# Performance work log

Hardware: AMD Instinct MI355X
Metric: run time of the kernel (lower is better)

Reference implementation:

```python
import jax, jax.numpy as jnp
import numpy as np

B, L, DIM, H, D = 4, 1024, 1024, 8, 32


def setup_inputs() -> dict:
    key = jax.random.key(0)
    ks = jax.random.split(key, 8)
    s = 0.02
    return dict(
        x=jax.random.normal(ks[0], (B, L, DIM), jnp.float32),
        W_in=jax.random.normal(ks[1], (DIM, DIM), jnp.float32) * s,
        b_in=jnp.zeros((DIM,), jnp.float32),
        W_qkva=jax.random.normal(ks[2], (H * D * 8, DIM), jnp.float32) * s,
        b_qkva=jnp.zeros((H * D * 8,), jnp.float32),
        W_y=jax.random.normal(ks[3], (DIM, H * D * 2), jnp.float32) * s,
        b_y=jnp.zeros((DIM,), jnp.float32),
        W_out=jax.random.normal(ks[4], (DIM, DIM), jnp.float32) * s,
        b_out=jnp.zeros((DIM,), jnp.float32),
        h0_re=jax.random.normal(ks[5], (H, D, D), jnp.float32),
        h0_im=jax.random.normal(ks[6], (H, D, D), jnp.float32),
    )


def reference(x, W_in, b_in, W_qkva, b_qkva, W_y, b_y, W_out, b_out, h0_re, h0_im):
    b, Ls, dim = x.shape
    Hh, Dd = h0_re.shape[0], h0_re.shape[1]
    u = jax.nn.silu(x @ W_in.T + b_in)
    qkva = (u @ W_qkva.T + b_qkva).reshape(b, Ls, Hh, Dd, 4, 2)
    c = jax.lax.complex(qkva[..., 0], qkva[..., 1])  # [b,L,H,D,4] complex
    q, k, v, a = c[..., 0], c[..., 1], c[..., 2], c[..., 3]
    mag2 = a.real * a.real + a.imag * a.imag
    # unit-modulus rotation scaled by sigmoid(log|a|^2) gate
    a = a * (jax.lax.rsqrt(mag2) * jax.nn.sigmoid(jnp.log(mag2)))
    kv = jnp.einsum('blhd,blhe->blhde', k, v)  # [b,L,H,D,D] complex
    h0 = jax.lax.complex(h0_re, h0_im)[None]  # [1,H,D,D]
    # fold initial state into step 0: h_0 = a_0 * h_init + kv_0
    kv = kv.at[:, 0].add(a[:, 0, ..., None] * h0)
    a_e = a[..., None]  # [b,L,H,D,1], broadcasts over state col dim

    def comb(c1, c2):
        a1, x1 = c1
        a2, x2 = c2
        return (a1 * a2, a2 * x1 + x2)

    # linear recurrence h_l = a_l * h_{l-1} + kv_l (equiv. to the FFT/cumsum
    # triangular-product matrix in the original module)
    _, h = jax.lax.associative_scan(comb, (a_e, kv), axis=1)
    y = jnp.einsum('blhd,blhde->blhe', q, h)  # [b,L,H,D] complex
    y2 = jnp.stack([y.real, y.imag], axis=-1).reshape(b, Ls, Hh * Dd * 2)
    y2 = jax.nn.silu(y2 @ W_y.T + b_y)
    return y2 @ W_out.T + b_out
```

## Files before the change

### kernel.cpp

```cpp
#include <hip/hip_runtime.h>

#define B_ 4
#define L_ 1024
#define DIM_ 1024
#define H_ 8
#define D_ 32
#define LSEG 16
#define NSEG (L_/LSEG)

typedef __bf16 bf16_t;
typedef __bf16 bf16x8 __attribute__((ext_vector_type(8)));
typedef float f32x4 __attribute__((ext_vector_type(4)));

__device__ __forceinline__ void gload_lds16(const bf16_t* g, bf16_t* l) {
  __builtin_amdgcn_global_load_lds((const __attribute__((address_space(1))) void*)g,
                                   (__attribute__((address_space(3))) void*)l, 16, 0, 0);
}
__device__ __forceinline__ void gload_lds16f(const float* g, float* l) {
  __builtin_amdgcn_global_load_lds((const __attribute__((address_space(1))) void*)g,
                                   (__attribute__((address_space(3))) void*)l, 16, 0, 0);
}

__global__ __launch_bounds__(256) void cvt_all(const float* __restrict__ x,
                                               const float* __restrict__ w1,
                                               const float* __restrict__ w2,
                                               const float* __restrict__ w3,
                                               const float* __restrict__ w4,
                                               bf16_t* __restrict__ ox,
                                               bf16_t* __restrict__ o1,
                                               bf16_t* __restrict__ o2,
                                               bf16_t* __restrict__ o3,
                                               bf16_t* __restrict__ o4) {
  int g = blockIdx.x;
  const float* in; bf16_t* out; int i;
  if      (g < 4096) { in = x;  out = ox; i = g * 256 + threadIdx.x; }
  else if (g < 5120) { in = w1; out = o1; i = (g - 4096) * 256 + threadIdx.x; }
  else if (g < 7168) { in = w2; out = o2; i = (g - 5120) * 256 + threadIdx.x; }
  else if (g < 7680) { in = w3; out = o3; i = (g - 7168) * 256 + threadIdx.x; }
  else               { in = w4; out = o4; i = (g - 7680) * 256 + threadIdx.x; }
  float4 v = ((const float4*)in)[i];
  union { bf16_t b[4]; unsigned long long q; } pk;
  pk.b[0] = (bf16_t)v.x; pk.b[1] = (bf16_t)v.y;
  pk.b[2] = (bf16_t)v.z; pk.b[3] = (bf16_t)v.w;
  ((unsigned long long*)out)[i] = pk.q;
}

template<int BN, int ACT, int OUTBF, int GATE, int TRANS>
__global__ __launch_bounds__(256) void gemm_nt(const bf16_t* __restrict__ A,
                                               const bf16_t* __restrict__ Bm,
                                               const float* __restrict__ bias,
                                               void* __restrict__ Cout,
                                               int M, int N, int K) {
  constexpr int NI = BN / 32;
  constexpr int ISS_B = BN / 32;
  __shared__ __align__(16) bf16_t As[128 * 64];
  __shared__ __align__(16) bf16_t Bs[BN * 64];
  const int t = threadIdx.x;
  const int wid = t >> 6, lane = t & 63;
  const int wr = wid >> 1, wc = wid & 1;
  const int lr = lane & 15, lq = lane >> 4;
  const int bm = blockIdx.x, bn = blockIdx.y;
  const int rA = wid * 32 + (lane >> 3);
  const int rB = wid * (BN / 4) + (lane >> 3);
  const int c8 = (((lane & 7) ^ ((lane >> 3) & 7))) * 8;
  const bf16_t* Ag = A + (size_t)(bm * 128 + rA) * K + c8;
  const bf16_t* Bg = Bm + (size_t)(bn * BN + rB) * K + c8;
  bf16_t* AsW = As + (wid * 32) * 64;
  bf16_t* BsW = Bs + (wid * (BN / 4)) * 64;
  f32x4 acc[4][NI] = {};
  for (int k0 = 0; k0 < K; k0 += 64) {
#pragma unroll
    for (int j = 0; j < 4; ++j)
      gload_lds16(Ag + (size_t)j * 8 * K, AsW + j * 8 * 64);
#pragma unroll
    for (int j = 0; j < ISS_B; ++j)
      gload_lds16(Bg + (size_t)j * 8 * K, BsW + j * 8 * 64);
    Ag += 64; Bg += 64;
    __syncthreads();
#pragma unroll
    for (int ks = 0; ks < 2; ++ks) {
      const int sg = ks * 4 + lq;
      const int sl = (sg ^ (lr & 7)) * 8;
      bf16x8 af[4], bfv[NI];
#pragma unroll
      for (int mi = 0; mi < 4; ++mi)
        af[mi] = *(const bf16x8*)&As[(wr * 64 + mi * 16 + lr) * 64 + sl];
#pragma unroll
      for (int ni = 0; ni < NI; ++ni)
        bfv[ni] = *(const bf16x8*)&Bs[(wc * (BN/2) + ni * 16 + lr) * 64 + sl];
#pragma unroll
      for (int mi = 0; mi < 4; ++mi)
#pragma unroll
        for (int ni = 0; ni < NI; ++ni)
          acc[mi][ni] = __builtin_amdgcn_mfma_f32_16x16x32_bf16(af[mi], bfv[ni], acc[mi][ni], 0, 0, 0);
    }
    __syncthreads();
  }
#pragma unroll
  for (int mi = 0; mi < 4; ++mi) {
#pragma unroll
    for (int ni = 0; ni < NI; ++ni) {
      int colg = bn * BN + wc * (BN/2) + ni * 16 + lr;
      float bb = bias[colg];
#pragma unroll
      for (int r = 0; r < 4; ++r) {
        int rowg = bm * 128 + wr * 64 + mi * 16 + lq * 4 + r;
        float v = acc[mi][ni][r] + bb;
        if (ACT == 1) v = v / (1.0f + __expf(-v));
        if (GATE) {
          float wv = __shfl_xor(v, 1);
          if ((colg & 7) >= 6) {
            float m2 = v * v + wv * wv;
            v *= sqrtf(m2) / (1.0f + m2);
          }
        }
        if (TRANS) {
          size_t idx = (((size_t)((rowg >> 10) * 8 + (colg >> 8))) * 1024
                        + (rowg & 1023)) * 256 + (colg & 255);
          ((float*)Cout)[idx] = v;
        } else if (OUTBF) {
          ((bf16_t*)Cout)[(size_t)rowg * N + colg] = (bf16_t)v;
        } else {
          ((float*)Cout)[(size_t)rowg * N + colg] = v;
        }
      }
    }
  }
}

template<int ACT, int OUTBF>
__global__ __launch_bounds__(256) void gemm_nt64(const bf16_t* __restrict__ A,
                                                 const bf16_t* __restrict__ Bm,
                                                 const float* __restrict__ bias,
                                                 void* __restrict__ Cout,
                                                 int M, int N, int K) {
  __shared__ __align__(16) bf16_t As[128 * 128];
  __shared__ __align__(16) bf16_t Bs[64 * 128];
  const int t = threadIdx.x;
  const int wid = t >> 6, lane = t & 63;
  const int wr = wid >> 1, wc = wid & 1;
  const int lr = lane & 15, lq = lane >> 4;
  const int bm = blockIdx.x, bn = blockIdx.y;
  const int crow = wid * 4 + (lane >> 4);
  const int c8 = ((lane & 15) ^ crow) * 8;
  const bf16_t* Ag = A + (size_t)(bm * 128 + crow) * K + c8;
  const bf16_t* Bg = Bm + (size_t)(bn * 64 + crow) * K + c8;
  bf16_t* AsW = As + (wid * 4) * 128;
  bf16_t* BsW = Bs + (wid * 4) * 128;
  f32x4 acc[4][2] = {};
  for (int k0 = 0; k0 < K; k0 += 128) {
#pragma unroll
    for (int j = 0; j < 8; ++j)
      gload_lds16(Ag + (size_t)j * 16 * K, AsW + j * 16 * 128);
#pragma unroll
    for (int j = 0; j < 4; ++j)
      gload_lds16(Bg + (size_t)j * 16 * K, BsW + j * 16 * 128);
    Ag += 128; Bg += 128;
    __syncthreads();
#pragma unroll
    for (int ks = 0; ks < 4; ++ks) {
      const int sg = ks * 4 + lq;
      const int sl = (sg ^ lr) * 8;
      bf16x8 af[4], bfv[2];
#pragma unroll
      for (int mi = 0; mi < 4; ++mi)
        af[mi] = *(const bf16x8*)&As[(wr * 64 + mi * 16 + lr) * 128 + sl];
#pragma unroll
      for (int ni = 0; ni < 2; ++ni)
        bfv[ni] = *(const bf16x8*)&Bs[(wc * 32 + ni * 16 + lr) * 128 + sl];
#pragma unroll
      for (int mi = 0; mi < 4; ++mi)
#pragma unroll
        for (int ni = 0; ni < 2; ++ni)
          acc[mi][ni] = __builtin_amdgcn_mfma_f32_16x16x32_bf16(af[mi], bfv[ni], acc[mi][ni], 0, 0, 0);
    }
    __syncthreads();
  }
#pragma unroll
  for (int mi = 0; mi < 4; ++mi) {
#pragma unroll
    for (int ni = 0; ni < 2; ++ni) {
      int colg = bn * 64 + wc * 32 + ni * 16 + lr;
      float bb = bias[colg];
#pragma unroll
      for (int r = 0; r < 4; ++r) {
        int rowg = bm * 128 + wr * 64 + mi * 16 + lq * 4 + r;
        float v = acc[mi][ni][r] + bb;
        if (ACT == 1) v = v / (1.0f + __expf(-v));
        if (OUTBF) ((bf16_t*)Cout)[(size_t)rowg * N + colg] = (bf16_t)v;
        else       ((float*)Cout)[(size_t)rowg * N + colg] = v;
      }
    }
  }
}

__global__ __launch_bounds__(256) void scan_seg(const float* __restrict__ qkvaT,
                                                float* __restrict__ y_loc,
                                                float* __restrict__ qP,
                                                float* __restrict__ Aseg,
                                                float* __restrict__ Hfin) {
  __shared__ __align__(16) float Q[LSEG * 256];
  const int t = threadIdx.x;
  const int seg = blockIdx.x;
  const int s = seg & (NSEG - 1);
  const int bh = seg >> 6;
  const int h = bh & (H_ - 1), b = bh >> 3;
  const int wid = t >> 6, lane = t & 63;
  const int dg = lane & 7, eh = lane >> 3;
  const int e = wid * 8 + eh;
  const float* gb = qkvaT + ((size_t)bh * L_ + s * LSEG) * 256;
#pragma unroll
  for (int c = 0; c < 4; ++c)
    gload_lds16f(gb + c * 1024 + t * 4, Q + c * 1024 + wid * 256);
  __syncthreads();
  float hr[4] = {}, hi[4] = {};
  float Pr[4] = {1,1,1,1}, Pi[4] = {0,0,0,0};
  size_t row = ((size_t)(b * L_ + s * LSEG) * H_ + h) * D_;
  for (int l = 0; l < LSEG; ++l) {
    const float* R = Q + l * 256;
    float2 vv = *(const float2*)(R + e * 8 + 4);
    float ytr = 0.f, yti = 0.f;
    float2 qpv[4];
#pragma unroll
    for (int j = 0; j < 4; ++j) {
      const int d = dg + 8 * j;
      float4 qk = *(const float4*)(R + d * 8);
      float2 aa = *(const float2*)(R + d * 8 + 6);
      float nPr = aa.x * Pr[j] - aa.y * Pi[j];
      float nPi = aa.x * Pi[j] + aa.y * Pr[j];
      Pr[j] = nPr; Pi[j] = nPi;
      qpv[j].x = qk.x * nPr - qk.y * nPi;
      qpv[j].y = qk.x * nPi + qk.y * nPr;
      float kvr = qk.z * vv.x - qk.w * vv.y;
      float kvi = qk.z * vv.y + qk.w * vv.x;
      float nhr = aa.x * hr[j] - aa.y * hi[j] + kvr;
      float nhi = aa.x * hi[j] + aa.y * hr[j] + kvi;
      hr[j] = nhr; hi[j] = nhi;
      ytr += qk.x * nhr - qk.y * nhi;
      yti += qk.x * nhi + qk.y * nhr;
    }
    ytr += __shfl_down(ytr, 4); yti += __shfl_down(yti, 4);
    ytr += __shfl_down(ytr, 2); yti += __shfl_down(yti, 2);
    ytr += __shfl_down(ytr, 1); yti += __shfl_down(yti, 1);
    if (dg == 0)
      *(float2*)(y_loc + (row + e) * 2) = make_float2(ytr, yti);
    if (t < 8) {
#pragma unroll
      for (int j = 0; j < 4; ++j)
        *(float2*)(qP + (row + dg + 8 * j) * 2) = qpv[j];
    }
    row += H_ * D_;
  }
  const size_t segb = (size_t)seg * D_;
  if (t < 8) {
#pragma unroll
    for (int j = 0; j < 4; ++j)
      *(float2*)(Aseg + (segb + dg + 8 * j) * 2) = make_float2(Pr[j], Pi[j]);
  }
#pragma unroll
  for (int j = 0; j < 4; ++j)
    *(float2*)(Hfin + ((segb + dg + 8 * j) * D_ + e) * 2) = make_float2(hr[j], hi[j]);
}

__global__ __launch_bounds__(128) void seg_combine(const float* __restrict__ h0re,
                                                   const float* __restrict__ h0im,
                                                   const float* __restrict__ Aseg,
                                                   const float* __restrict__ Hfin,
                                                   float* __restrict__ Hc) {
  const int bh = blockIdx.x >> 3;
  const int eg = blockIdx.x & 7;
  const int h = bh & (H_ - 1);
  const int t = threadIdx.x;
  const int d = t >> 2;
  const int e = eg * 4 + (t & 3);
  float cr = h0re[((size_t)h * D_ + d) * D_ + e];
  float ci = h0im[((size_t)h * D_ + d) * D_ + e];
  size_t idx = ((size_t)bh * NSEG * D_ + d) * D_ + e;
  size_t aidx = (size_t)bh * NSEG * D_ + d;
  float2 A0 = *(const float2*)(Aseg + aidx * 2);
  float2 F0 = *(const float2*)(Hfin + idx * 2);
  for (int s = 0; s < NSEG; ++s) {
    float2 A1, F1;
    if (s + 1 < NSEG) {
      A1 = *(const float2*)(Aseg + (aidx + D_) * 2);
      F1 = *(const float2*)(Hfin + (idx + D_ * D_) * 2);
    }
    *(float2*)(Hc + idx * 2) = make_float2(cr, ci);
    float nr = A0.x * cr - A0.y * ci + F0.x;
    float ni = A0.x * ci + A0.y * cr + F0.y;
    cr = nr; ci = ni;
    A0 = A1; F0 = F1;
    idx += D_ * D_; aidx += D_;
  }
}

__global__ __launch_bounds__(256) void y_correct(const float* __restrict__ y_loc,
                                                 const float* __restrict__ qP,
                                                 const float* __restrict__ Hc,
                                                 bf16_t* __restrict__ y2b) {
  __shared__ __align__(16) float Hs[D_ * D_ * 2];
  const int seg = blockIdx.x;
  const int s = seg & (NSEG - 1);
  const int bh = seg >> 6;
  const int h = bh & (H_ - 1), b = bh >> 3;
  const int t = threadIdx.x;
  const float4* src = (const float4*)(Hc + (size_t)seg * (D_ * D_ * 2));
  ((float4*)Hs)[t] = src[t];
  ((float4*)Hs)[t + 256] = src[t + 256];
  __syncthreads();
  const int l = t >> 4;
  const int ep = (t & 15) * 2;
  const int lg = s * LSEG + l;
  const size_t rowc = ((size_t)(b * L_ + lg) * H_ + h) * D_;
  const float* qpr = qP + rowc * 2;
  float4 y0 = *(const float4*)(y_loc + (rowc + ep) * 2);
  float ac_r[2] = {y0.x, y0.z}, ac_i[2] = {y0.y, y0.w};
#pragma unroll 4
  for (int d = 0; d < D_; ++d) {
    float2 p = *(const float2*)(qpr + d * 2);
    float4 hv = *(const float4*)&Hs[(d * D_ + ep) * 2];
    ac_r[0] += p.x * hv.x - p.y * hv.y; ac_i[0] += p.x * hv.y + p.y * hv.x;
    ac_r[1] += p.x * hv.z - p.y * hv.w; ac_i[1] += p.x * hv.w + p.y * hv.z;
  }
  union { bf16_t bv[4]; uint2 q; } pk;
  pk.bv[0] = (bf16_t)ac_r[0]; pk.bv[1] = (bf16_t)ac_i[0];
  pk.bv[2] = (bf16_t)ac_r[1]; pk.bv[3] = (bf16_t)ac_i[1];
  *(uint2*)(y2b + (size_t)(b * L_ + lg) * (H_ * D_ * 2) + (h * D_ + ep) * 2) = pk.q;
}

extern "C" void kernel_launch(void* const* d_in, const int* in_sizes, int n_in,
                              void* d_out, int out_size, void* d_ws, size_t ws_size,
                              hipStream_t stream) {
  const float* x      = (const float*)d_in[0];
  const float* W_in   = (const float*)d_in[1];
  const float* b_in   = (const float*)d_in[2];
  const float* W_qkva = (const float*)d_in[3];
  const float* b_qkva = (const float*)d_in[4];
  const float* W_y    = (const float*)d_in[5];
  const float* b_y    = (const float*)d_in[6];
  const float* W_out  = (const float*)d_in[7];
  const float* b_out  = (const float*)d_in[8];
  const float* h0re   = (const float*)d_in[9];
  const float* h0im   = (const float*)d_in[10];

  char* w = (char*)d_ws;
  const size_t MB = 1ull << 20;
  bf16_t* Wb_in   = (bf16_t*)(w + 0*MB);
  bf16_t* Wb_qkva = (bf16_t*)(w + 2*MB);
  bf16_t* Wb_y    = (bf16_t*)(w + 6*MB);
  bf16_t* Wb_out  = (bf16_t*)(w + 7*MB);
  bf16_t* xb      = (bf16_t*)(w + 9*MB);
  float*  qP      = (float*) (w + 9*MB);
  bf16_t* u       = (bf16_t*)(w + 17*MB);
  float*  y_loc   = (float*) (w + 17*MB);
  float*  qkvaT   = (float*) (w + 25*MB);
  float*  Hc      = (float*) (w + 25*MB);
  bf16_t* y2b     = (bf16_t*)(w + 41*MB);
  bf16_t* z       = (bf16_t*)(w + 45*MB);
  float*  Aseg    = (float*) (w + 57*MB);
  float*  Hfin    = (float*) (w + 58*MB);

  cvt_all<<<8704, 256, 0, stream>>>(x, W_in, W_qkva, W_y, W_out,
                                    xb, Wb_in, Wb_qkva, Wb_y, Wb_out);

  gemm_nt64<1,1><<<dim3(32, 16), 256, 0, stream>>>(xb, Wb_in, b_in, u, 4096, 1024, 1024);
  gemm_nt<128,0,0,1,1><<<dim3(32, 16), 256, 0, stream>>>(u, Wb_qkva, b_qkva, qkvaT, 4096, 2048, 1024);
  scan_seg   <<<2048, 256, 0, stream>>>(qkvaT, y_loc, qP, Aseg, Hfin);
  seg_combine<<<256,  128, 0, stream>>>(h0re, h0im, Aseg, Hfin, Hc);
  y_correct  <<<2048, 256, 0, stream>>>(y_loc, qP, Hc, y2b);
  gemm_nt64<1,1><<<dim3(32, 16), 256, 0, stream>>>(y2b, Wb_y, b_y, z, 4096, 1024, 512);
  gemm_nt64<0,0><<<dim3(32, 16), 256, 0, stream>>>(z, Wb_out, b_out, (float*)d_out, 4096, 1024, 1024);
}
```

Before: 229.7 us.

## Store qkva row-major and gather per-head rows in scan; deepen combine prefetch

The qkva GEMM now writes its fp32 output in plain row-major order instead of a per-(batch,head) transposed layout. The segment scan kernel compensates by loading each time step's 256-float head slice with strided global-to-LDS loads. Separately, seg_combine keeps an 8-deep register prefetch buffer of segment decay and state values instead of 1-deep, to hide load latency in its serial recurrence. The aim is to cut the scattered epilogue stores in the GEMM and to raise memory-level parallelism in the combine step, at the cost of less contiguous reads in the scan.

New measurement: 226.2 us. Within noise of the previous version (-1.5%).

```diff
diff --git a/kernel.cpp b/kernel.cpp
--- a/kernel.cpp
+++ b/kernel.cpp
@@ -45,7 +45,7 @@
   ((unsigned long long*)out)[i] = pk.q;
 }
 
-template<int BN, int ACT, int OUTBF, int GATE, int TRANS>
+template<int BN, int ACT, int OUTBF, int GATE>
 __global__ __launch_bounds__(256) void gemm_nt(const bf16_t* __restrict__ A,
                                                const bf16_t* __restrict__ Bm,
                                                const float* __restrict__ bias,
@@ -114,15 +114,8 @@
             v *= sqrtf(m2) / (1.0f + m2);
           }
         }
-        if (TRANS) {
-          size_t idx = (((size_t)((rowg >> 10) * 8 + (colg >> 8))) * 1024
-                        + (rowg & 1023)) * 256 + (colg & 255);
-          ((float*)Cout)[idx] = v;
-        } else if (OUTBF) {
-          ((bf16_t*)Cout)[(size_t)rowg * N + colg] = (bf16_t)v;
-        } else {
-          ((float*)Cout)[(size_t)rowg * N + colg] = v;
-        }
+        if (OUTBF) ((bf16_t*)Cout)[(size_t)rowg * N + colg] = (bf16_t)v;
+        else       ((float*)Cout)[(size_t)rowg * N + colg] = v;
       }
     }
   }
@@ -194,7 +187,7 @@
   }
 }
 
-__global__ __launch_bounds__(256) void scan_seg(const float* __restrict__ qkvaT,
+__global__ __launch_bounds__(256) void scan_seg(const float* __restrict__ qkva,
                                                 float* __restrict__ y_loc,
                                                 float* __restrict__ qP,
                                                 float* __restrict__ Aseg,
@@ -208,10 +201,12 @@
   const int wid = t >> 6, lane = t & 63;
   const int dg = lane & 7, eh = lane >> 3;
   const int e = wid * 8 + eh;
-  const float* gb = qkvaT + ((size_t)bh * L_ + s * LSEG) * 256;
-#pragma unroll
-  for (int c = 0; c < 4; ++c)
-    gload_lds16f(gb + c * 1024 + t * 4, Q + c * 1024 + wid * 256);
+  const float* gb = qkva + ((size_t)(b * L_ + s * LSEG) * H_ + h) * 256;
+#pragma unroll
+  for (int j = 0; j < 4; ++j) {
+    const int l = wid * 4 + j;
+    gload_lds16f(gb + (size_t)l * (H_ * 256) + lane * 4, Q + l * 256);
+  }
   __syncthreads();
   float hr[4] = {}, hi[4] = {};
   float Pr[4] = {1,1,1,1}, Pi[4] = {0,0,0,0};
@@ -275,22 +270,28 @@
   const int e = eg * 4 + (t & 3);
   float cr = h0re[((size_t)h * D_ + d) * D_ + e];
   float ci = h0im[((size_t)h * D_ + d) * D_ + e];
-  size_t idx = ((size_t)bh * NSEG * D_ + d) * D_ + e;
-  size_t aidx = (size_t)bh * NSEG * D_ + d;
-  float2 A0 = *(const float2*)(Aseg + aidx * 2);
-  float2 F0 = *(const float2*)(Hfin + idx * 2);
-  for (int s = 0; s < NSEG; ++s) {
-    float2 A1, F1;
-    if (s + 1 < NSEG) {
-      A1 = *(const float2*)(Aseg + (aidx + D_) * 2);
-      F1 = *(const float2*)(Hfin + (idx + D_ * D_) * 2);
-    }
-    *(float2*)(Hc + idx * 2) = make_float2(cr, ci);
-    float nr = A0.x * cr - A0.y * ci + F0.x;
-    float ni = A0.x * ci + A0.y * cr + F0.y;
-    cr = nr; ci = ni;
-    A0 = A1; F0 = F1;
-    idx += D_ * D_; aidx += D_;
+  const size_t idx0  = ((size_t)bh * NSEG * D_ + d) * D_ + e;
+  const size_t aidx0 = (size_t)bh * NSEG * D_ + d;
+  float2 Ab[8], Fb[8];
+#pragma unroll
+  for (int p = 0; p < 8; ++p) {
+    Ab[p] = *(const float2*)(Aseg + (aidx0 + (size_t)p * D_) * 2);
+    Fb[p] = *(const float2*)(Hfin + (idx0 + (size_t)p * D_ * D_) * 2);
+  }
+  for (int so = 0; so < NSEG; so += 8) {
+#pragma unroll
+    for (int p = 0; p < 8; ++p) {
+      const int s = so + p;
+      float2 A0 = Ab[p], F0 = Fb[p];
+      if (so + 8 < NSEG) {
+        Ab[p] = *(const float2*)(Aseg + (aidx0 + (size_t)(s + 8) * D_) * 2);
+        Fb[p] = *(const float2*)(Hfin + (idx0 + (size_t)(s + 8) * D_ * D_) * 2);
+      }
+      *(float2*)(Hc + (idx0 + (size_t)s * D_ * D_) * 2) = make_float2(cr, ci);
+      float nr = A0.x * cr - A0.y * ci + F0.x;
+      float ni = A0.x * ci + A0.y * cr + F0.y;
+      cr = nr; ci = ni;
+    }
   }
 }
 
@@ -353,7 +354,7 @@
   float*  qP      = (float*) (w + 9*MB);
   bf16_t* u       = (bf16_t*)(w + 17*MB);
   float*  y_loc   = (float*) (w + 17*MB);
-  float*  qkvaT   = (float*) (w + 25*MB);
+  float*  qkva    = (float*) (w + 25*MB);
   float*  Hc      = (float*) (w + 25*MB);
   bf16_t* y2b     = (bf16_t*)(w + 41*MB);
   bf16_t* z       = (bf16_t*)(w + 45*MB);
@@ -364,8 +365,8 @@
                                     xb, Wb_in, Wb_qkva, Wb_y, Wb_out);
 
   gemm_nt64<1,1><<<dim3(32, 16), 256, 0, stream>>>(xb, Wb_in, b_in, u, 4096, 1024, 1024);
-  gemm_nt<128,0,0,1,1><<<dim3(32, 16), 256, 0, stream>>>(u, Wb_qkva, b_qkva, qkvaT, 4096, 2048, 1024);
-  scan_seg   <<<2048, 256, 0, stream>>>(qkvaT, y_loc, qP, Aseg, Hfin);
+  gemm_nt<128,0,0,1><<<dim3(32, 16), 256, 0, stream>>>(u, Wb_qkva, b_qkva, qkva, 4096, 2048, 1024);
+  scan_seg   <<<2048, 256, 0, stream>>>(qkva, y_loc, qP, Aseg, Hfin);
   seg_combine<<<256,  128, 0, stream>>>(h0re, h0im, Aseg, Hfin, Hc);
   y_correct  <<<2048, 256, 0, stream>>>(y_loc, qP, Hc, y2b);
   gemm_nt64<1,1><<<dim3(32, 16), 256, 0, stream>>>(y2b, Wb_y, b_y, z, 4096, 1024, 512);
```
